# Performance work log

Hardware: AMD Instinct MI355X
Metric: run time of the kernel (lower is better)

## Reference

```python
import jax, jax.numpy as jnp
import numpy as np

IN_CH = 128
OUT_CH = 32
HEADS = 4
N_NODES = 50000
N_EDGES = 500000
NEG_SLOPE = 0.01  # torch leaky_relu default


def setup_inputs() -> dict:
    key = jax.random.key(0)
    ks = jax.random.split(key, 8)
    E, D, H, C = N_EDGES, IN_CH, HEADS, OUT_CH
    receivers = jax.random.normal(ks[0], (E, D), dtype=jnp.float32)
    senders = jax.random.normal(ks[1], (E, D), dtype=jnp.float32)
    edge_attribute = jax.random.normal(ks[2], (E, D), dtype=jnp.float32)
    sender_idx = jax.random.randint(ks[3], (E,), 0, N_NODES)
    receiver_idx = jax.random.randint(ks[4], (E,), 0, N_NODES)
    # bias-free linear weights, stored as [in, heads*out] so y = x @ W
    scale = 1.0 / np.sqrt(D)
    W_src = jax.random.normal(ks[5], (D, H * C), dtype=jnp.float32) * scale
    W_tgt = jax.random.normal(ks[6], (D, H * C), dtype=jnp.float32) * scale
    W_edge = jax.random.normal(ks[7], (D, H * C), dtype=jnp.float32) * scale
    # xavier_normal_ on shape (1, H, C): std = sqrt(2/(H + C)) per torch fan calc on last two dims
    attn = jax.random.normal(jax.random.fold_in(key, 99), (1, H, C), dtype=jnp.float32) * np.sqrt(2.0 / (H + C))
    return {
        "receivers": receivers,
        "senders": senders,
        "edge_attribute": edge_attribute,
        "sender_idx": sender_idx,
        "receiver_idx": receiver_idx,
        "W_src": W_src,
        "W_tgt": W_tgt,
        "W_edge": W_edge,
        "attn": attn,
    }


def reference(receivers, senders, edge_attribute, sender_idx, receiver_idx, W_src, W_tgt, W_edge, attn):
    E = receivers.shape[0]
    H, C = HEADS, OUT_CH
    t = (receivers @ W_tgt).reshape(E, H, C)   # target projection of receiver feats
    s = (senders @ W_src).reshape(E, H, C)
    e = (edge_attribute @ W_edge).reshape(E, H, C)
    z = (jax.nn.leaky_relu(s + t + e, NEG_SLOPE) * attn).sum(-1)  # [E, H]
    # segment softmax over edges grouped by sender_idx
    zmax = jax.ops.segment_max(z, sender_idx, num_segments=N_NODES)  # [N, H]
    ez = jnp.exp(z - zmax[sender_idx])
    denom = jax.ops.segment_sum(ez, sender_idx, num_segments=N_NODES)
    a = ez / denom[sender_idx]                 # [E, H]
    m = t * a[..., None]                        # [E, H, C]
    aggr_m = jax.ops.segment_sum(m, receiver_idx, num_segments=N_NODES)  # [N, H, C]
    return aggr_m.mean(axis=1), m.mean(axis=1)  # ([N, C], [E, C])
```

## Files before the change

kernel.cpp:

```cpp
#include <hip/hip_runtime.h>
#include <hip/hip_bf16.h>

#define E_EDGES 500000
#define NN 50000

typedef unsigned short u16;
typedef __attribute__((ext_vector_type(8))) short s16x8;
typedef __attribute__((ext_vector_type(4))) float f32x4;

#define BAR() __builtin_amdgcn_s_barrier()
#define SCHED0() __builtin_amdgcn_sched_barrier(0)
#define WAITLGKM0() asm volatile("s_waitcnt lgkmcnt(0)" ::: "memory")

__device__ __forceinline__ short f2bf(float f) {
    unsigned u = __builtin_bit_cast(unsigned, f);
    u += 0x7fffu + ((u >> 16) & 1u);
    return (short)(u >> 16);
}

__device__ __forceinline__ float lrelu(float x) { return x > 0.0f ? x : 0.01f * x; }

__device__ __forceinline__ s16x8 cvt8(float4 lo, float4 hi) {
    union { s16x8 v; __hip_bfloat162 h[4]; } u;
    u.h[0] = __float22bfloat162_rn(make_float2(lo.x, lo.y));
    u.h[1] = __float22bfloat162_rn(make_float2(lo.z, lo.w));
    u.h[2] = __float22bfloat162_rn(make_float2(hi.x, hi.y));
    u.h[3] = __float22bfloat162_rn(make_float2(hi.z, hi.w));
    return u.v;
}

__global__ void kprep(const float* __restrict__ Wsrc, const float* __restrict__ Wtgt,
                      const float* __restrict__ Wedge, u16* __restrict__ WT) {
    int i = blockIdx.x * 256 + threadIdx.x;
    if (i >= 3 * 16384) return;
    int g = i >> 14, nk = i & 16383, n = nk >> 7, k = nk & 127;
    const float* W = (g == 0) ? Wsrc : (g == 1) ? Wtgt : Wedge;
    WT[i] = (u16)f2bf(W[k * 128 + n]);
}

__global__ __launch_bounds__(256, 2) void k1(
    const float* __restrict__ recv, const float* __restrict__ send,
    const float* __restrict__ eattr, const int* __restrict__ sidx,
    const u16* __restrict__ WT, const float* __restrict__ attn,
    float* __restrict__ ez, float* __restrict__ denom)
{
    __shared__ u16 ldsA[3][64][136];
    __shared__ float smEz[64][4];
    const int tid = threadIdx.x;
    const int lane = tid & 63, wv = tid >> 6;
    const int l15 = lane & 15, lg = (lane >> 4) & 3;

    const float* Xg[3] = {send, eattr, recv};
    const int bgoff[3] = {0, 2 * 16384, 1 * 16384};

    s16x8 bfr[3][4][2];
#pragma unroll
    for (int g = 0; g < 3; ++g)
#pragma unroll
        for (int kk = 0; kk < 4; ++kk)
#pragma unroll
            for (int nn = 0; nn < 2; ++nn)
                bfr[g][kk][nn] = *(const s16x8*)(WT + bgoff[g] +
                    ((wv * 2 + nn) * 16 + l15) * 128 + kk * 32 + lg * 8);

    const float av0 = attn[(wv * 2 + 0) * 16 + l15];
    const float av1 = attn[(wv * 2 + 1) * 16 + l15];

    f32x4 acc[4][2];
    float4 ra[12][2];

    auto issueA = [&](int tileRow) {
#pragma unroll
        for (int q = 0; q < 12; ++q) {
            int idx = tid + 256 * q;
            int mat = idx >> 10, rem = idx & 1023;
            int row = rem >> 4, gcol = (rem & 15) * 8;
            int ge = min(tileRow + row, E_EDGES - 1);
            const float* p = Xg[mat] + (size_t)ge * 128 + gcol;
            ra[q][0] = *(const float4*)p;
            ra[q][1] = *(const float4*)(p + 4);
        }
    };

    auto commitA = [&]() {
#pragma unroll
        for (int q = 0; q < 12; ++q) {
            int idx = tid + 256 * q;
            int mat = idx >> 10, rem = idx & 1023;
            *(s16x8*)&ldsA[mat][rem >> 4][(rem & 15) * 8] = cvt8(ra[q][0], ra[q][1]);
        }
    };

    const int b = blockIdx.x;
    const int row0 = b * 64;

    issueA(row0);
    SCHED0();
    commitA();
    WAITLGKM0();
    BAR();

#pragma unroll
    for (int m = 0; m < 4; ++m)
#pragma unroll
        for (int nn = 0; nn < 2; ++nn) acc[m][nn] = (f32x4){0.f, 0.f, 0.f, 0.f};

#pragma unroll
    for (int g = 0; g < 3; ++g) {
#pragma unroll
        for (int kk = 0; kk < 4; ++kk) {
            int k0 = kk * 32 + lg * 8;
#pragma unroll
            for (int m = 0; m < 4; ++m) {
                s16x8 a = *(const s16x8*)&ldsA[g][m * 16 + l15][k0];
                acc[m][0] = __builtin_amdgcn_mfma_f32_16x16x32_bf16(a, bfr[g][kk][0], acc[m][0], 0, 0, 0);
                acc[m][1] = __builtin_amdgcn_mfma_f32_16x16x32_bf16(a, bfr[g][kk][1], acc[m][1], 0, 0, 0);
            }
        }
    }

#pragma unroll
    for (int m = 0; m < 4; ++m) {
        float part[4];
#pragma unroll
        for (int j = 0; j < 4; ++j)
            part[j] = lrelu(acc[m][0][j]) * av0 + lrelu(acc[m][1][j]) * av1;
#pragma unroll
        for (int off = 1; off < 16; off <<= 1) {
#pragma unroll
            for (int j = 0; j < 4; ++j) part[j] += __shfl_xor(part[j], off, 64);
        }
        if (l15 == 0) {
#pragma unroll
            for (int j = 0; j < 4; ++j)
                smEz[m * 16 + lg * 4 + j][wv] = __expf(part[j]);
        }
    }
    __syncthreads();
    {
        int row = tid >> 2, h = tid & 3;
        int r = row0 + row;
        float v = smEz[row][h];
        if (r < E_EDGES) {
            ez[(size_t)r * 4 + h] = v;
            int s = sidx[r];
            atomicAdd(&denom[(size_t)s * 4 + h], v);
        }
    }
}

__global__ __launch_bounds__(256, 2) void k2(
    const float* __restrict__ recv, const int* __restrict__ ridx,
    const int* __restrict__ sidx, const u16* __restrict__ WTt,
    const float* __restrict__ ez, const float* __restrict__ denom,
    float* __restrict__ out0, float* __restrict__ out1)
{
    __shared__ u16 ldsA[64][136];
    __shared__ u16 ldsB[128][136];
    const int tid = threadIdx.x;
    const int lane = tid & 63, wv = tid >> 6;
    const int l15 = lane & 15, lg = (lane >> 4) & 3;
    const int row0 = blockIdx.x * 64;

    float4 ra[4][2];
#pragma unroll
    for (int q = 0; q < 4; ++q) {
        int idx = tid + 256 * q;
        int row = idx >> 4, gcol = (idx & 15) * 8;
        int ge = min(row0 + row, E_EDGES - 1);
        const float* p = recv + (size_t)ge * 128 + gcol;
        ra[q][0] = *(const float4*)p;
        ra[q][1] = *(const float4*)(p + 4);
    }
    s16x8 rb[8];
#pragma unroll
    for (int q = 0; q < 8; ++q) {
        int idx = tid + 256 * q;
        rb[q] = *(const s16x8*)(WTt + (idx >> 4) * 128 + (idx & 15) * 8);
    }
#pragma unroll
    for (int q = 0; q < 4; ++q) {
        int idx = tid + 256 * q;
        *(s16x8*)&ldsA[idx >> 4][(idx & 15) * 8] = cvt8(ra[q][0], ra[q][1]);
    }
#pragma unroll
    for (int q = 0; q < 8; ++q) {
        int idx = tid + 256 * q;
        *(s16x8*)&ldsB[idx >> 4][(idx & 15) * 8] = rb[q];
    }
    __syncthreads();

    f32x4 acc[8];
#pragma unroll
    for (int n = 0; n < 8; ++n) acc[n] = (f32x4){0.f, 0.f, 0.f, 0.f};

#pragma unroll
    for (int kk = 0; kk < 4; ++kk) {
        int k0 = kk * 32 + lg * 8;
        s16x8 a = *(const s16x8*)&ldsA[wv * 16 + l15][k0];
#pragma unroll
        for (int n = 0; n < 8; ++n) {
            s16x8 b = *(const s16x8*)&ldsB[n * 16 + l15][k0];
            acc[n] = __builtin_amdgcn_mfma_f32_16x16x32_bf16(a, b, acc[n], 0, 0, 0);
        }
    }

#pragma unroll
    for (int j = 0; j < 4; ++j) {
        int r = row0 + wv * 16 + lg * 4 + j;
        if (r < E_EDGES) {
            int s = sidx[r];
            float4 ezv = *(const float4*)(ez + (size_t)r * 4);
            float4 dn = *(const float4*)(denom + (size_t)s * 4);
            float a0 = ezv.x / dn.x, a1 = ezv.y / dn.y;
            float a2 = ezv.z / dn.z, a3 = ezv.w / dn.w;
            float lo = 0.25f * (acc[0][j] * a0 + acc[2][j] * a1 +
                                acc[4][j] * a2 + acc[6][j] * a3);
            float hi = 0.25f * (acc[1][j] * a0 + acc[3][j] * a1 +
                                acc[5][j] * a2 + acc[7][j] * a3);
            out1[(size_t)r * 32 + l15] = lo;
            out1[(size_t)r * 32 + 16 + l15] = hi;
            int rv = ridx[r];
            atomicAdd(&out0[(size_t)rv * 32 + l15], lo);
            atomicAdd(&out0[(size_t)rv * 32 + 16 + l15], hi);
        }
    }
}

extern "C" void kernel_launch(void* const* d_in, const int* in_sizes, int n_in,
                              void* d_out, int out_size, void* d_ws, size_t ws_size,
                              hipStream_t stream) {
    const float* recv  = (const float*)d_in[0];
    const float* send  = (const float*)d_in[1];
    const float* eattr = (const float*)d_in[2];
    const int*   sidx  = (const int*)d_in[3];
    const int*   ridx  = (const int*)d_in[4];
    const float* Wsrc  = (const float*)d_in[5];
    const float* Wtgt  = (const float*)d_in[6];
    const float* Wedge = (const float*)d_in[7];
    const float* attn  = (const float*)d_in[8];

    char* ws = (char*)d_ws;
    u16*   WT    = (u16*)ws;
    float* ez    = (float*)(ws + 131072);
    float* denom = (float*)(ws + 131072 + 8000000);

    float* out0 = (float*)d_out;
    float* out1 = out0 + (size_t)NN * 32;

    hipMemsetAsync(denom, 0, (size_t)NN * 4 * sizeof(float), stream);
    hipMemsetAsync(out0, 0, (size_t)NN * 32 * sizeof(float), stream);

    kprep<<<192, 256, 0, stream>>>(Wsrc, Wtgt, Wedge, WT);

    int nb = (E_EDGES + 63) / 64;
    k1<<<nb, 256, 0, stream>>>(recv, send, eattr, sidx, WT, attn, ez, denom);
    k2<<<nb, 256, 0, stream>>>(recv, ridx, sidx, WT + 16384, ez, denom, out0, out1);
}
```

Measured before the change: 307.0 us.

## Stream k1 inputs via async global_load_lds with double-buffered fp32 LDS

The k1 kernel now uses direct global-to-LDS async loads (global_load_lds, 16 bytes each) into a two-slot fp32 LDS buffer with an XOR swizzle. The three input matrices are pipelined, so the next matrix loads while MFMAs run on the current one. Conversion to bf16 moves to LDS read time. This removes the register staging and explicit convert-and-store pass and overlaps memory with compute. In exchange it doubles LDS bytes per element, adds conversion work inside the MFMA loop, and relies on hand-placed vmcnt waits, including one that drains the weight loads up front.

```diff
diff --git a/kernel.cpp b/kernel.cpp
--- a/kernel.cpp
+++ b/kernel.cpp
@@ -10,7 +10,7 @@
 
 #define BAR() __builtin_amdgcn_s_barrier()
 #define SCHED0() __builtin_amdgcn_sched_barrier(0)
-#define WAITLGKM0() asm volatile("s_waitcnt lgkmcnt(0)" ::: "memory")
+#define WAITVM(N) asm volatile("s_waitcnt vmcnt(" #N ")" ::: "memory")
 
 __device__ __forceinline__ short f2bf(float f) {
     unsigned u = __builtin_bit_cast(unsigned, f);
@@ -29,6 +29,12 @@
     return u.v;
 }
 
+__device__ __forceinline__ void gll16(const float* g, const float* l) {
+    __builtin_amdgcn_global_load_lds(
+        (const __attribute__((address_space(1))) unsigned*)g,
+        (__attribute__((address_space(3))) unsigned*)l, 16, 0, 0);
+}
+
 __global__ void kprep(const float* __restrict__ Wsrc, const float* __restrict__ Wtgt,
                       const float* __restrict__ Wedge, u16* __restrict__ WT) {
     int i = blockIdx.x * 256 + threadIdx.x;
@@ -44,11 +50,12 @@
     const u16* __restrict__ WT, const float* __restrict__ attn,
     float* __restrict__ ez, float* __restrict__ denom)
 {
-    __shared__ u16 ldsA[3][64][136];
+    __shared__ float ldsA[2][64][128];
     __shared__ float smEz[64][4];
     const int tid = threadIdx.x;
     const int lane = tid & 63, wv = tid >> 6;
     const int l15 = lane & 15, lg = (lane >> 4) & 3;
+    const int row0 = blockIdx.x * 64;
 
     const float* Xg[3] = {send, eattr, recv};
     const int bgoff[3] = {0, 2 * 16384, 1 * 16384};
@@ -65,58 +72,55 @@
 
     const float av0 = attn[(wv * 2 + 0) * 16 + l15];
     const float av1 = attn[(wv * 2 + 1) * 16 + l15];
+    WAITVM(0);
+    SCHED0();
+
+    auto issue = [&](const float* X, int buf) {
+#pragma unroll
+        for (int q = 0; q < 8; ++q) {
+            int row = wv * 16 + q * 2 + (lane >> 5);
+            int gsrc = (lane & 31) ^ (row & 7);
+            int grow = min(row0 + row, E_EDGES - 1);
+            const float* gp = X + (size_t)grow * 128 + gsrc * 4;
+            gll16(gp, &ldsA[buf][0][0] + (wv * 512 + q * 64) * 4);
+        }
+    };
 
     f32x4 acc[4][2];
-    float4 ra[12][2];
-
-    auto issueA = [&](int tileRow) {
-#pragma unroll
-        for (int q = 0; q < 12; ++q) {
-            int idx = tid + 256 * q;
-            int mat = idx >> 10, rem = idx & 1023;
-            int row = rem >> 4, gcol = (rem & 15) * 8;
-            int ge = min(tileRow + row, E_EDGES - 1);
-            const float* p = Xg[mat] + (size_t)ge * 128 + gcol;
-            ra[q][0] = *(const float4*)p;
-            ra[q][1] = *(const float4*)(p + 4);
+#pragma unroll
+    for (int m = 0; m < 4; ++m)
+#pragma unroll
+        for (int nn = 0; nn < 2; ++nn) acc[m][nn] = (f32x4){0.f, 0.f, 0.f, 0.f};
+
+    auto mfma_ph = [&](int buf, const s16x8 (&bf)[4][2]) {
+#pragma unroll
+        for (int kk = 0; kk < 4; ++kk) {
+#pragma unroll
+            for (int m = 0; m < 4; ++m) {
+                int row = m * 16 + l15;
+                int gr0 = kk * 8 + lg * 2, sw = row & 7;
+                const float* rp = &ldsA[buf][row][0];
+                float4 lo = *(const float4*)(rp + ((gr0 ^ sw) * 4));
+                float4 hi = *(const float4*)(rp + (((gr0 + 1) ^ sw) * 4));
+                s16x8 a = cvt8(lo, hi);
+                acc[m][0] = __builtin_amdgcn_mfma_f32_16x16x32_bf16(a, bf[kk][0], acc[m][0], 0, 0, 0);
+                acc[m][1] = __builtin_amdgcn_mfma_f32_16x16x32_bf16(a, bf[kk][1], acc[m][1], 0, 0, 0);
+            }
         }
     };
 
-    auto commitA = [&]() {
-#pragma unroll
-        for (int q = 0; q < 12; ++q) {
-            int idx = tid + 256 * q;
-            int mat = idx >> 10, rem = idx & 1023;
-            *(s16x8*)&ldsA[mat][rem >> 4][(rem & 15) * 8] = cvt8(ra[q][0], ra[q][1]);
-        }
-    };
-
-    const int b = blockIdx.x;
-    const int row0 = b * 64;
-
-    issueA(row0);
-    SCHED0();
-    commitA();
-    WAITLGKM0();
-    BAR();
-
-#pragma unroll
-    for (int m = 0; m < 4; ++m)
-#pragma unroll
-        for (int nn = 0; nn < 2; ++nn) acc[m][nn] = (f32x4){0.f, 0.f, 0.f, 0.f};
-
+    issue(Xg[0], 0);
+    int buf = 0;
 #pragma unroll
     for (int g = 0; g < 3; ++g) {
-#pragma unroll
-        for (int kk = 0; kk < 4; ++kk) {
-            int k0 = kk * 32 + lg * 8;
-#pragma unroll
-            for (int m = 0; m < 4; ++m) {
-                s16x8 a = *(const s16x8*)&ldsA[g][m * 16 + l15][k0];
-                acc[m][0] = __builtin_amdgcn_mfma_f32_16x16x32_bf16(a, bfr[g][kk][0], acc[m][0], 0, 0, 0);
-                acc[m][1] = __builtin_amdgcn_mfma_f32_16x16x32_bf16(a, bfr[g][kk][1], acc[m][1], 0, 0, 0);
-            }
-        }
+        if (g == 0) { issue(Xg[1], 1); WAITVM(8); }
+        else if (g == 1) { issue(Xg[2], 0); WAITVM(8); }
+        else { WAITVM(0); }
+        BAR(); SCHED0();
+        mfma_ph(buf, bfr[g]);
+        SCHED0();
+        BAR();
+        buf ^= 1;
     }
 
 #pragma unroll
```

After: 310.9 us. Within noise of the previous version (+1.3%).
